# Optimization experiments

Measured on AMD Instinct MI355X. Metric: run time of the kernel, lower is better.

## Reference

```python
import jax, jax.numpy as jnp
import numpy as np

B, L, D_MODEL, D_K = 4, 2048, 1024, 128


def setup_inputs() -> dict:
    key = jax.random.key(0)
    ks = jax.random.split(key, 4)
    scale = 1.0 / np.sqrt(D_MODEL)
    x = jax.random.normal(ks[0], (B, L, D_MODEL), dtype=jnp.float32)
    Wq = jax.random.normal(ks[1], (D_MODEL, D_K), dtype=jnp.float32) * scale
    Wk = jax.random.normal(ks[2], (D_MODEL, D_K), dtype=jnp.float32) * scale
    Wv = jax.random.normal(ks[3], (D_MODEL, D_K), dtype=jnp.float32) * scale
    bq = jnp.zeros((D_K,), dtype=jnp.float32)
    bk = jnp.zeros((D_K,), dtype=jnp.float32)
    bv = jnp.zeros((D_K,), dtype=jnp.float32)
    return {"x": x, "Wq": Wq, "bq": bq, "Wk": Wk, "bk": bk, "Wv": Wv, "bv": bv}


def reference(x, Wq, bq, Wk, bk, Wv, bv):
    # Dense projections (keras Dense = xW + b)
    Q = jnp.einsum("bld,dk->blk", x, Wq) + bq  # [B, L, d_k]
    K = jnp.einsum("bld,dk->blk", x, Wk) + bk
    V = jnp.einsum("bld,dk->blk", x, Wv) + bv
    QK = jnp.einsum("blk,bmk->blm", Q, K)      # [B, L, L]
    # Original: real( complex(cos(QK), sin(QK)) @ complex(V, 0) )
    # Since imag(V) == 0, the real part is exactly cos(QK) @ V; the sin
    # branch contributes only to the discarded imaginary part.
    out = jnp.einsum("blm,bmk->blk", jnp.cos(QK), V)  # [B, L, d_k]
    return out
```

## Files before the change

### kernel.cpp

```cpp
#include <hip/hip_runtime.h>

typedef _Float16 half8_t __attribute__((ext_vector_type(8)));
typedef _Float16 half4_t __attribute__((ext_vector_type(4)));
typedef __attribute__((ext_vector_type(4))) float float4_t;

#define MFMA16 __builtin_amdgcn_mfma_f32_16x16x32_f16

constexpr int BB   = 4;
constexpr int LL   = 2048;
constexpr int DM   = 1024;
constexpr int DK   = 128;
constexpr int MTOT = BB * LL;
constexpr int MC   = 4;
constexpr float INV2PI = 0.15915494309189535f;

__device__ __forceinline__ void gload16(const void* g, void* l) {
    __builtin_amdgcn_global_load_lds(
        (const __attribute__((address_space(1))) void*)g,
        (__attribute__((address_space(3))) void*)l, 16, 0, 0);
}

__global__ __launch_bounds__(256) void k0_wsplit(
        const float* __restrict__ wq, const float* __restrict__ wk,
        const float* __restrict__ wv,
        _Float16* __restrict__ wq6, _Float16* __restrict__ wk6,
        _Float16* __restrict__ wv6) {
    int kc = blockIdx.x, a = blockIdx.y;
    const float* w = (a == 0) ? wq : (a == 1) ? wk : wv;
    _Float16* dst = (a == 0) ? wq6 : (a == 1) ? wk6 : wv6;
    __shared__ float tile[64 * 132];
    int t = threadIdx.x;
#pragma unroll
    for (int j = 0; j < 8; ++j) {
        int idx4 = t + j * 256;
        int kr = idx4 >> 5, n4 = idx4 & 31;
        *(float4_t*)(&tile[kr * 132 + n4 * 4]) =
            *(const float4_t*)(w + (size_t)(kc * 64 + kr) * DK + n4 * 4);
    }
    __syncthreads();
#pragma unroll
    for (int sw = 0; sw < 4; ++sw) {
        int ch = t + sw * 256;
        int cbt = ch >> 7, s = (ch >> 4) & 7, cc = ch & 15;
        int kb = (s >> 2) * 32 + (s & 3) * 8;
        int n = cbt * 16 + cc;
        half8_t h;
#pragma unroll
        for (int e = 0; e < 8; ++e) h[e] = (_Float16)tile[(kb + e) * 132 + n];
        *(half8_t*)(dst + (size_t)kc * 8192 + ch * 8) = h;
    }
}

__global__ __launch_bounds__(256, 3) void k1_proj(
        const float* __restrict__ x,
        const float* __restrict__ bq, const float* __restrict__ bk,
        const float* __restrict__ bv,
        const _Float16* __restrict__ wq6, const _Float16* __restrict__ wk6,
        const _Float16* __restrict__ wv6,
        _Float16* __restrict__ qim, _Float16* __restrict__ kim,
        _Float16* __restrict__ vim) {
    int mt = blockIdx.x, grp = blockIdx.y;
    int rowbase = mt * 32;
    __shared__ __attribute__((aligned(16))) _Float16 xs[2][32 * 72];
    __shared__ __attribute__((aligned(16))) _Float16 wsm[2][8192];

    int t = threadIdx.x, lane = t & 63, wid = t >> 6;
    int cc = lane & 15, g = lane >> 4;
    const _Float16* W6 = (grp == 0) ? wq6 : (grp == 1) ? wk6 : wv6;

    float4_t acc[2][2];
#pragma unroll
    for (int rf = 0; rf < 2; ++rf)
#pragma unroll
        for (int cf = 0; cf < 2; ++cf) acc[rf][cf] = (float4_t){0.f, 0.f, 0.f, 0.f};

    int xr = t >> 3, xc8 = t & 7;
    const float* xsrc = x + (size_t)(rowbase + xr) * DM + xc8 * 8;
    int xoff = xr * 72 + xc8 * 8;

    auto stageW = [&](int kc, int buf) {
        const _Float16* Wp = W6 + (size_t)kc * 8192;
#pragma unroll
        for (int i = 0; i < 4; ++i)
            gload16(Wp + i * 2048 + t * 8, (char*)wsm[buf] + i * 4096 + wid * 1024);
    };
    auto cvt8 = [&](float4_t f0, float4_t f1) {
        half8_t h;
#pragma unroll
        for (int e = 0; e < 4; ++e) { h[e] = (_Float16)f0[e]; h[e + 4] = (_Float16)f1[e]; }
        return h;
    };

    {
        float4_t f0 = *(const float4_t*)(xsrc);
        float4_t f1 = *(const float4_t*)(xsrc + 4);
        stageW(0, 0);
        *(half8_t*)(xs[0] + xoff) = cvt8(f0, f1);
    }
    __syncthreads();

#pragma unroll 1
    for (int kc = 0; kc < 16; ++kc) {
        int cb = kc & 1, nb = cb ^ 1;
        bool more = (kc < 15);
        float4_t f0, f1;
        if (more) {
            f0 = *(const float4_t*)(xsrc + (size_t)(kc + 1) * 64);
            f1 = *(const float4_t*)(xsrc + (size_t)(kc + 1) * 64 + 4);
            stageW(kc + 1, nb);
        }
        half8_t a_[2][2], b_[2][2];
#pragma unroll
        for (int rf = 0; rf < 2; ++rf)
#pragma unroll
            for (int ks = 0; ks < 2; ++ks)
                a_[rf][ks] = *(const half8_t*)(xs[cb] + (rf * 16 + cc) * 72 + ks * 32 + g * 8);
#pragma unroll
        for (int cf = 0; cf < 2; ++cf)
#pragma unroll
            for (int ks = 0; ks < 2; ++ks)
                b_[cf][ks] = *(const half8_t*)(wsm[cb] + (wid * 2 + cf) * 1024 +
                                               (ks * 4 + g) * 128 + cc * 8);
#pragma unroll
        for (int cf = 0; cf < 2; ++cf)
#pragma unroll
            for (int rf = 0; rf < 2; ++rf) {
                acc[rf][cf] = MFMA16(a_[rf][0], b_[cf][0], acc[rf][cf], 0, 0, 0);
                acc[rf][cf] = MFMA16(a_[rf][1], b_[cf][1], acc[rf][cf], 0, 0, 0);
            }
        if (more) *(half8_t*)(xs[nb] + xoff) = cvt8(f0, f1);
        __syncthreads();
    }

    const float* bias = (grp == 0) ? bq : (grp == 1) ? bk : bv;
#pragma unroll
    for (int rf = 0; rf < 2; ++rf)
#pragma unroll
        for (int cf = 0; cf < 2; ++cf) {
            int c = wid * 32 + cf * 16 + cc;
            float bv_ = bias[c];
#pragma unroll
            for (int i = 0; i < 4; ++i) {
                int r = rowbase + rf * 16 + g * 4 + i;
                float v = acc[rf][cf][i] + bv_;
                if (grp == 0) {
                    size_t o = (size_t)(r >> 4) * 2048 + (c >> 5) * 512 +
                               ((c >> 3) & 3) * 128 + (r & 15) * 8 + (c & 7);
                    qim[o] = (_Float16)v;
                } else if (grp == 1) {
                    size_t o = (size_t)(r >> 5) * 4096 + ((r >> 4) & 1) * 2048 +
                               (c >> 5) * 512 + ((c >> 3) & 3) * 128 +
                               (r & 15) * 8 + (c & 7);
                    kim[o] = (_Float16)v;
                } else {
                    size_t o = (size_t)(r >> 5) * 4096 + (c >> 4) * 512 +
                               ((r >> 3) & 3) * 128 + (c & 15) * 8 + (r & 7);
                    vim[o] = (_Float16)v;
                }
            }
        }
}

__global__ __launch_bounds__(256, 2) void k2_attn(
        const _Float16* __restrict__ qim, const _Float16* __restrict__ kim,
        const _Float16* __restrict__ vim, _Float16* __restrict__ part) {
    int mc = blockIdx.x, qt = blockIdx.y, b = blockIdx.z;
    int t = threadIdx.x, lane = t & 63, wid = t >> 6;
    int cc = lane & 15, g = lane >> 4;

    __shared__ __attribute__((aligned(16))) _Float16 kb[2][8192];
    __shared__ __attribute__((aligned(16))) _Float16 vb[2][8192];
    __shared__ __attribute__((aligned(16))) _Float16 ps[4][1024];

    int qrow = b * LL + qt * 64 + wid * 16;
    const _Float16* qb_ = qim + (size_t)(qrow >> 4) * 2048;
    half8_t qf[4];
#pragma unroll
    for (int s = 0; s < 4; ++s)
        qf[s] = *(const half8_t*)(qb_ + s * 512 + g * 128 + cc * 8);

    float4_t o[8];
#pragma unroll
    for (int cf = 0; cf < 8; ++cf) o[cf] = (float4_t){0.f, 0.f, 0.f, 0.f};

    int tbase = b * 64 + mc * 16;

    auto stageKV = [&](int mi, int buf) {
        const _Float16* ks = kim + (size_t)(tbase + mi * 2) * 4096;
        const _Float16* vs = vim + (size_t)(tbase + mi * 2) * 4096;
#pragma unroll
        for (int i = 0; i < 4; ++i) {
            gload16(ks + i * 2048 + t * 8, (char*)kb[buf] + i * 4096 + wid * 1024);
            gload16(vs + i * 2048 + t * 8, (char*)vb[buf] + i * 4096 + wid * 1024);
        }
    };

    stageKV(0, 0);
    __syncthreads();

#pragma unroll 1
    for (int mi = 0; mi < 8; ++mi) {
        int cb = mi & 1, nb = cb ^ 1;
        if (mi < 7) stageKV(mi + 1, nb);
        float4_t sa[4];
#pragma unroll
        for (int cf = 0; cf < 4; ++cf) sa[cf] = (float4_t){0.f, 0.f, 0.f, 0.f};
#pragma unroll
        for (int cf = 0; cf < 4; ++cf)
#pragma unroll
            for (int s = 0; s < 4; ++s) {
                half8_t kf = *(const half8_t*)(kb[cb] + cf * 2048 + s * 512 +
                                               g * 128 + cc * 8);
                sa[cf] = MFMA16(kf, qf[s], sa[cf], 0, 0, 0);
            }
#pragma unroll
        for (int cf = 0; cf < 4; ++cf) {
            half4_t h4;
#pragma unroll
            for (int i = 0; i < 4; ++i) {
                float rv = sa[cf][i] * INV2PI;
                rv = rv - floorf(rv);
                float cv;
                asm volatile("v_cos_f32 %0, %1" : "=v"(cv) : "v"(rv));
                h4[i] = (_Float16)cv;
            }
            int base = (cf * 2 + (g >> 1)) * 128 + cc * 8 + (g & 1) * 4;
            *(half4_t*)(&ps[wid][base]) = h4;
        }
#pragma unroll
        for (int ksv = 0; ksv < 2; ++ksv) {
            half8_t pa = *(const half8_t*)(&ps[wid][(ksv * 4 + g) * 128 + cc * 8]);
#pragma unroll
            for (int cf = 0; cf < 8; ++cf) {
                half8_t vbf = *(const half8_t*)(vb[cb] + ksv * 4096 + cf * 512 +
                                                g * 128 + cc * 8);
                o[cf] = MFMA16(pa, vbf, o[cf], 0, 0, 0);
            }
        }
        __syncthreads();
    }
    _Float16* pp = part + ((size_t)(mc * BB + b) * LL + qt * 64 + wid * 16) * DK;
#pragma unroll
    for (int cf = 0; cf < 8; ++cf)
#pragma unroll
        for (int i = 0; i < 4; ++i)
            pp[(g * 4 + i) * DK + cf * 16 + cc] = (_Float16)o[cf][i];
}

__global__ __launch_bounds__(256) void k3_reduce(const _Float16* __restrict__ part,
                                                 float4_t* __restrict__ out) {
    constexpr int NT8 = MTOT * DK / 8;
    int idx = blockIdx.x * 256 + threadIdx.x;
    const half8_t* p = (const half8_t*)part;
    float s[8];
#pragma unroll
    for (int e = 0; e < 8; ++e) s[e] = 0.f;
#pragma unroll
    for (int c = 0; c < MC; ++c) {
        half8_t v = p[idx + (size_t)c * NT8];
#pragma unroll
        for (int e = 0; e < 8; ++e) s[e] += (float)v[e];
    }
    float4_t o0 = {s[0], s[1], s[2], s[3]};
    float4_t o1 = {s[4], s[5], s[6], s[7]};
    out[idx * 2]     = o0;
    out[idx * 2 + 1] = o1;
}

extern "C" void kernel_launch(void* const* d_in, const int* in_sizes, int n_in,
                              void* d_out, int out_size, void* d_ws, size_t ws_size,
                              hipStream_t stream) {
    const float* x  = (const float*)d_in[0];
    const float* Wq = (const float*)d_in[1];
    const float* bq = (const float*)d_in[2];
    const float* Wk = (const float*)d_in[3];
    const float* bk = (const float*)d_in[4];
    const float* Wv = (const float*)d_in[5];
    const float* bv = (const float*)d_in[6];

    char* ws = (char*)d_ws;
    size_t off = 0;
    auto alloc = [&](size_t bytes) -> char* {
        char* p = ws + off;
        off += (bytes + 255) & ~(size_t)255;
        return p;
    };
    _Float16* wq6 = (_Float16*)alloc((size_t)DK * DM * 2);
    _Float16* wk6 = (_Float16*)alloc((size_t)DK * DM * 2);
    _Float16* wv6 = (_Float16*)alloc((size_t)DK * DM * 2);
    _Float16* qim = (_Float16*)alloc((size_t)MTOT * DK * 2);
    _Float16* kim = (_Float16*)alloc((size_t)MTOT * DK * 2);
    _Float16* vim = (_Float16*)alloc((size_t)MTOT * DK * 2);
    _Float16* part = (_Float16*)alloc((size_t)MC * MTOT * DK * 2);

    k0_wsplit<<<dim3(16, 3), 256, 0, stream>>>(Wq, Wk, Wv, wq6, wk6, wv6);
    k1_proj<<<dim3(MTOT / 32, 3), 256, 0, stream>>>(x, bq, bk, bv,
                                                    wq6, wk6, wv6, qim, kim, vim);
    k2_attn<<<dim3(MC, LL / 64, BB), 256, 0, stream>>>(qim, kim, vim, part);
    k3_reduce<<<(MTOT * DK / 8) / 256, 256, 0, stream>>>(part, (float4_t*)d_out);
}
```

Before: 47.41 us.

## Switch attention kernel to 32x32x16 MFMA with new Q/K/V layouts

Rewrites the attention kernel to use 32x32x16 f16 MFMA instead of 16x16x32. Each wave now handles 32 query rows, and each block handles 128 query rows. The projection kernel writes Q, K and V in new interleaved layouts that match the 32x32 operand fragments. The key dimension is split into 8 chunks instead of 4, with 32-key tiles per step, to keep the grid size the same. This aims to cut LDS reads and instruction count per FLOP. The cost is writing and then reducing twice as many fp16 partial outputs in the reduce kernel.

After: 48.96 us. 1.03x slower.

```diff
diff --git a/kernel.cpp b/kernel.cpp
--- a/kernel.cpp
+++ b/kernel.cpp
@@ -3,15 +3,17 @@
 typedef _Float16 half8_t __attribute__((ext_vector_type(8)));
 typedef _Float16 half4_t __attribute__((ext_vector_type(4)));
 typedef __attribute__((ext_vector_type(4))) float float4_t;
+typedef __attribute__((ext_vector_type(16))) float float16_t;
 
 #define MFMA16 __builtin_amdgcn_mfma_f32_16x16x32_f16
+#define MFMA32 __builtin_amdgcn_mfma_f32_32x32x16_f16
 
 constexpr int BB   = 4;
 constexpr int LL   = 2048;
 constexpr int DM   = 1024;
 constexpr int DK   = 128;
 constexpr int MTOT = BB * LL;
-constexpr int MC   = 4;
+constexpr int MC   = 8;
 constexpr float INV2PI = 0.15915494309189535f;
 
 __device__ __forceinline__ void gload16(const void* g, void* l) {
@@ -19,6 +21,7 @@
         (const __attribute__((address_space(1))) void*)g,
         (__attribute__((address_space(3))) void*)l, 16, 0, 0);
 }
+
 
 __global__ __launch_bounds__(256) void k0_wsplit(
         const float* __restrict__ wq, const float* __restrict__ wk,
@@ -143,18 +146,14 @@
             for (int i = 0; i < 4; ++i) {
                 int r = rowbase + rf * 16 + g * 4 + i;
                 float v = acc[rf][cf][i] + bv_;
-                if (grp == 0) {
-                    size_t o = (size_t)(r >> 4) * 2048 + (c >> 5) * 512 +
-                               ((c >> 3) & 3) * 128 + (r & 15) * 8 + (c & 7);
-                    qim[o] = (_Float16)v;
-                } else if (grp == 1) {
-                    size_t o = (size_t)(r >> 5) * 4096 + ((r >> 4) & 1) * 2048 +
-                               (c >> 5) * 512 + ((c >> 3) & 3) * 128 +
-                               (r & 15) * 8 + (c & 7);
-                    kim[o] = (_Float16)v;
+                if (grp <= 1) {
+                    size_t o = (size_t)(r >> 5) * 4096 + (c >> 4) * 512 +
+                               (size_t)((r & 31) + 32 * ((c >> 3) & 1)) * 8 + (c & 7);
+                    ((grp == 0) ? qim : kim)[o] = (_Float16)v;
                 } else {
-                    size_t o = (size_t)(r >> 5) * 4096 + (c >> 4) * 512 +
-                               ((r >> 3) & 3) * 128 + (c & 15) * 8 + (r & 7);
+                    size_t o = (size_t)(r >> 5) * 4096 + (c >> 5) * 1024 +
+                               ((r >> 4) & 1) * 512 +
+                               (size_t)((c & 31) + 32 * ((r >> 3) & 1)) * 8 + (r & 7);
                     vim[o] = (_Float16)v;
                 }
             }
@@ -166,30 +165,31 @@
         const _Float16* __restrict__ vim, _Float16* __restrict__ part) {
     int mc = blockIdx.x, qt = blockIdx.y, b = blockIdx.z;
     int t = threadIdx.x, lane = t & 63, wid = t >> 6;
-    int cc = lane & 15, g = lane >> 4;
-
-    __shared__ __attribute__((aligned(16))) _Float16 kb[2][8192];
-    __shared__ __attribute__((aligned(16))) _Float16 vb[2][8192];
+
+    __shared__ __attribute__((aligned(16))) _Float16 kb[2][4096];
+    __shared__ __attribute__((aligned(16))) _Float16 vb[2][4096];
     __shared__ __attribute__((aligned(16))) _Float16 ps[4][1024];
 
-    int qrow = b * LL + qt * 64 + wid * 16;
-    const _Float16* qb_ = qim + (size_t)(qrow >> 4) * 2048;
-    half8_t qf[4];
-#pragma unroll
-    for (int s = 0; s < 4; ++s)
-        qf[s] = *(const half8_t*)(qb_ + s * 512 + g * 128 + cc * 8);
-
-    float4_t o[8];
-#pragma unroll
-    for (int cf = 0; cf < 8; ++cf) o[cf] = (float4_t){0.f, 0.f, 0.f, 0.f};
-
-    int tbase = b * 64 + mc * 16;
+    int qrow0 = b * LL + qt * 128 + wid * 32;
+    const _Float16* qb_ = qim + (size_t)(qrow0 >> 5) * 4096;
+    half8_t qf[8];
+#pragma unroll
+    for (int s = 0; s < 8; ++s)
+        qf[s] = *(const half8_t*)(qb_ + s * 512 + lane * 8);
+
+    float16_t o[4];
+#pragma unroll
+    for (int dt = 0; dt < 4; ++dt)
+#pragma unroll
+        for (int e = 0; e < 16; ++e) o[dt][e] = 0.f;
+
+    int tbase = b * 64 + mc * 8;
 
     auto stageKV = [&](int mi, int buf) {
-        const _Float16* ks = kim + (size_t)(tbase + mi * 2) * 4096;
-        const _Float16* vs = vim + (size_t)(tbase + mi * 2) * 4096;
-#pragma unroll
-        for (int i = 0; i < 4; ++i) {
+        const _Float16* ks = kim + (size_t)(tbase + mi) * 4096;
+        const _Float16* vs = vim + (size_t)(tbase + mi) * 4096;
+#pragma unroll
+        for (int i = 0; i < 2; ++i) {
             gload16(ks + i * 2048 + t * 8, (char*)kb[buf] + i * 4096 + wid * 1024);
             gload16(vs + i * 2048 + t * 8, (char*)vb[buf] + i * 4096 + wid * 1024);
         }
@@ -202,49 +202,49 @@
     for (int mi = 0; mi < 8; ++mi) {
         int cb = mi & 1, nb = cb ^ 1;
         if (mi < 7) stageKV(mi + 1, nb);
-        float4_t sa[4];
-#pragma unroll
-        for (int cf = 0; cf < 4; ++cf) sa[cf] = (float4_t){0.f, 0.f, 0.f, 0.f};
-#pragma unroll
-        for (int cf = 0; cf < 4; ++cf)
-#pragma unroll
-            for (int s = 0; s < 4; ++s) {
-                half8_t kf = *(const half8_t*)(kb[cb] + cf * 2048 + s * 512 +
-                                               g * 128 + cc * 8);
-                sa[cf] = MFMA16(kf, qf[s], sa[cf], 0, 0, 0);
-            }
-#pragma unroll
-        for (int cf = 0; cf < 4; ++cf) {
+        float16_t sa;
+#pragma unroll
+        for (int e = 0; e < 16; ++e) sa[e] = 0.f;
+#pragma unroll
+        for (int s = 0; s < 8; ++s) {
+            half8_t kf = *(const half8_t*)(kb[cb] + s * 512 + lane * 8);
+            sa = MFMA32(kf, qf[s], sa, 0, 0, 0);
+        }
+#pragma unroll
+        for (int j = 0; j < 4; ++j) {
             half4_t h4;
 #pragma unroll
             for (int i = 0; i < 4; ++i) {
-                float rv = sa[cf][i] * INV2PI;
+                float rv = sa[4 * j + i] * INV2PI;
                 rv = rv - floorf(rv);
                 float cv;
                 asm volatile("v_cos_f32 %0, %1" : "=v"(cv) : "v"(rv));
                 h4[i] = (_Float16)cv;
             }
-            int base = (cf * 2 + (g >> 1)) * 128 + cc * 8 + (g & 1) * 4;
-            *(half4_t*)(&ps[wid][base]) = h4;
-        }
-#pragma unroll
-        for (int ksv = 0; ksv < 2; ++ksv) {
-            half8_t pa = *(const half8_t*)(&ps[wid][(ksv * 4 + g) * 128 + cc * 8]);
-#pragma unroll
-            for (int cf = 0; cf < 8; ++cf) {
-                half8_t vbf = *(const half8_t*)(vb[cb] + ksv * 4096 + cf * 512 +
-                                                g * 128 + cc * 8);
-                o[cf] = MFMA16(pa, vbf, o[cf], 0, 0, 0);
+            int m0 = 8 * j + 4 * (lane >> 5);
+            int addr = (m0 >> 4) * 512 + ((lane & 31) + 32 * ((m0 >> 3) & 1)) * 8 +
+                       (m0 & 7);
+            *(half4_t*)(&ps[wid][addr]) = h4;
+        }
+#pragma unroll
+        for (int ms = 0; ms < 2; ++ms) {
+            half8_t pa = *(const half8_t*)(&ps[wid][ms * 512 + lane * 8]);
+#pragma unroll
+            for (int dt = 0; dt < 4; ++dt) {
+                half8_t vf = *(const half8_t*)(vb[cb] + (dt * 2 + ms) * 512 + lane * 8);
+                o[dt] = MFMA32(pa, vf, o[dt], 0, 0, 0);
             }
         }
         __syncthreads();
     }
-    _Float16* pp = part + ((size_t)(mc * BB + b) * LL + qt * 64 + wid * 16) * DK;
-#pragma unroll
-    for (int cf = 0; cf < 8; ++cf)
-#pragma unroll
-        for (int i = 0; i < 4; ++i)
-            pp[(g * 4 + i) * DK + cf * 16 + cc] = (_Float16)o[cf][i];
+    _Float16* pp = part + ((size_t)(mc * BB + b) * LL + qt * 128 + wid * 32) * DK;
+#pragma unroll
+    for (int dt = 0; dt < 4; ++dt)
+#pragma unroll
+        for (int reg = 0; reg < 16; ++reg) {
+            int q = (reg & 3) + 8 * (reg >> 2) + 4 * (lane >> 5);
+            pp[q * DK + dt * 32 + (lane & 31)] = (_Float16)o[dt][reg];
+        }
 }
 
 __global__ __launch_bounds__(256) void k3_reduce(const _Float16* __restrict__ part,
@@ -296,6 +296,6 @@
     k0_wsplit<<<dim3(16, 3), 256, 0, stream>>>(Wq, Wk, Wv, wq6, wk6, wv6);
     k1_proj<<<dim3(MTOT / 32, 3), 256, 0, stream>>>(x, bq, bk, bv,
                                                     wq6, wk6, wv6, qim, kim, vim);
-    k2_attn<<<dim3(MC, LL / 64, BB), 256, 0, stream>>>(qim, kim, vim, part);
+    k2_attn<<<dim3(MC, LL / 128, BB), 256, 0, stream>>>(qim, kim, vim, part);
     k3_reduce<<<(MTOT * DK / 8) / 256, 256, 0, stream>>>(part, (float4_t*)d_out);
 }
```
